# Performance work log

Hardware: AMD Instinct MI355X
Metric: run time of the kernel (lower is better)

Reference implementation:

```python
import jax, jax.numpy as jnp
import numpy as np

B, T, D, N = 16, 4096, 512, 3


def _window_sum(x, k):
    # x: [B, T, ...] -> sliding-window sum of size k, stride 1 -> [B, T-k+1, ...]
    c = jnp.cumsum(x, axis=1)
    c = jnp.concatenate([jnp.zeros_like(c[:, :1]), c], axis=1)
    return c[:, k:] - c[:, :-k]


def setup_inputs() -> dict:
    key = jax.random.key(0)
    ks = jax.random.split(key, 7)
    s_prev = jax.random.normal(ks[0], (B, D), jnp.float32)
    enc_hs = jax.random.normal(ks[1], (B, T, D), jnp.float32)
    # realistic padding mask: True = padded position
    lengths = jax.random.randint(ks[2], (B,), T // 2, T + 1)
    src_mask = jnp.arange(T)[None, :] >= lengths[:, None]
    scale = 1.0 / np.sqrt(D)
    Vw = jax.random.normal(ks[3], (N, D, D), jnp.float32) * scale
    Vb = jax.random.normal(ks[4], (N, D), jnp.float32) * 0.01
    Ww = jax.random.normal(ks[5], (N, D, D), jnp.float32) * scale
    Wb = jax.random.normal(ks[6], (N, D), jnp.float32) * 0.01
    return {"s_prev": s_prev, "enc_hs": enc_hs, "src_mask": src_mask,
            "Vw": Vw, "Vb": Vb, "Ww": Ww, "Wb": Wb}


def _level(s_prev, hs, mask, vw, vb, ww, wb):
    # hs: [B, L, D], mask: [B, L] (True = masked)
    # torch Linear: y = x @ W^T + b, weight is [out, in]
    v = jnp.einsum('bld,ed->ble', hs, vw) + vb            # V_i(hs)
    att = jnp.einsum('bd,bld->bl', s_prev, v)             # bmm(s_prev, V(hs)^T)
    att = jnp.where(mask, -jnp.inf, att)
    att = jax.nn.softmax(att, axis=-1)                    # [B, L]
    pooled = jnp.einsum('bl,bld->bd', att, hs)            # bmm(att, hs)
    ctx = pooled @ ww.T + wb                              # W_i(.)
    return ctx, att


def reference(s_prev, enc_hs, src_mask, Vw, Vb, Ww, Wb):
    ctx, att = _level(s_prev, enc_hs, src_mask, Vw[0], Vb[0], Ww[0], Wb[0])
    for i in range(1, N):
        k = i + 1
        hs_ngram = _window_sum(enc_hs, k) / k                      # AvgPool1d(k,1)
        n_mask = _window_sum(src_mask.astype(jnp.float32), k) > 0  # any masked in window
        c, _ = _level(s_prev, hs_ngram, n_mask, Vw[i], Vb[i], Ww[i], Wb[i])
        ctx = ctx + c
    return ctx, att
```

## Files before the change

kernel.cpp:

```cpp
#include <hip/hip_runtime.h>

#define BB 16
#define TT 4096
#define DD 512
#define CH 32
#define GR 4
#define NG (TT/(CH*GR))
#define NEG (-1.0e30f)

#define OFF_Q     64
#define OFF_QP    (OFF_Q + 3*BB*DD)
#define OFF_P0    (OFF_QP + 8*3*BB*DD)
#define OFF_M     (OFF_P0 + BB*TT)
#define OFF_S     (OFF_M + 3*BB*NG)
#define OFF_MT    (OFF_S + 3*BB*NG)
#define OFF_TOT   (OFF_MT + 64)
#define OFF_PART  (OFF_TOT + 64)
#define OFF_POOL  (OFF_PART + 3*NG*BB*DD)

__global__ void __launch_bounds__(256) k_pre(const unsigned char* __restrict__ mask,
                                             const float* __restrict__ s_prev,
                                             const float* __restrict__ Vw,
                                             int* __restrict__ lengths,
                                             float* __restrict__ qpart) {
    const int tid = threadIdx.x;
    if (blockIdx.x < BB) {
        __shared__ int sflag;
        __shared__ int wsum[4];
        const int b = blockIdx.x;
        if (tid == 0) sflag = 0;
        __syncthreads();
        const uint4* m4 = (const uint4*)mask;
        int f = 0;
        #pragma unroll 4
        for (int idx = tid; idx < BB * TT / 16; idx += 256) {
            const uint4 w = m4[idx];
            f |= (((w.x | w.y | w.z | w.w) & 0xFFFFFF00u) != 0u);
        }
        if (f) atomicOr(&sflag, 1);
        __syncthreads();
        const bool byte_layout = (sflag != 0);
        const int* m32 = (const int*)mask;
        int cnt = 0;
        if (byte_layout) {
            for (int t = tid; t < TT; t += 256) cnt += (mask[b * TT + t] != 0);
        } else {
            for (int t = tid; t < TT; t += 256) cnt += (m32[b * TT + t] != 0);
        }
        #pragma unroll
        for (int m = 32; m >= 1; m >>= 1) cnt += __shfl_xor(cnt, m, 64);
        if ((tid & 63) == 0) wsum[tid >> 6] = cnt;
        __syncthreads();
        if (tid == 0) lengths[b] = TT - (wsum[0] + wsum[1] + wsum[2] + wsum[3]);
    } else {
        __shared__ float4 red[2][128];
        const int idx = blockIdx.x - BB;
        const int ib = idx >> 3;
        const int ec = idx & 7;
        const int b = ib % BB;
        const int i = ib / BB;
        const int es = tid >> 7;
        const int dq = tid & 127;
        const int e0 = ec * 64 + es * 32;
        const float* sp = s_prev + b * DD + e0;
        const float4* W = (const float4*)(Vw + (size_t)i * DD * DD + (size_t)e0 * DD) + dq;
        float4 acc = make_float4(0.f, 0.f, 0.f, 0.f);
        #pragma unroll 8
        for (int e = 0; e < 32; e++) {
            const float sev = sp[e];
            const float4 w = W[e * 128];
            acc.x += sev * w.x; acc.y += sev * w.y;
            acc.z += sev * w.z; acc.w += sev * w.w;
        }
        red[es][dq] = acc;
        __syncthreads();
        if (tid < 128) {
            const float4 r0 = red[0][tid], r1 = red[1][tid];
            const float4 o = make_float4(r0.x + r1.x, r0.y + r1.y,
                                         r0.z + r1.z, r0.w + r1.w);
            ((float4*)(qpart + (size_t)idx * DD))[tid] = o;
        }
    }
}

__global__ void __launch_bounds__(256) k_q2(const float* __restrict__ qpart,
                                            float* __restrict__ q) {
    const int idx = blockIdx.x * 256 + threadIdx.x;
    const int ib = idx / DD;
    const int d = idx % DD;
    float s = 0.f;
    #pragma unroll
    for (int ec = 0; ec < 8; ec++) s += qpart[(size_t)(ib * 8 + ec) * DD + d];
    q[idx] = s;
}

__global__ void __launch_bounds__(512, 4) k_fused(const float* __restrict__ enc,
                                                  const float* __restrict__ q,
                                                  const int* __restrict__ lengths,
                                                  float* __restrict__ p0,
                                                  float* __restrict__ mbuf,
                                                  float* __restrict__ sbuf,
                                                  float* __restrict__ part) {
    __shared__ float se[CH + 2][DD];
    __shared__ float sp[CH + 2][3];
    __shared__ float su[3][CH];
    __shared__ float sms[3], sss[3];
    const int b = blockIdx.x;
    const int g = blockIdx.y;
    const int t0g = g * (CH * GR);
    const int len = lengths[b];
    const int tid = threadIdx.x;
    if (t0g >= len) {
        if (tid < 3) {
            mbuf[(size_t)(tid * BB + b) * NG + g] = NEG;
            sbuf[(size_t)(tid * BB + b) * NG + g] = 0.f;
        }
        return;
    }
    const int wv = tid >> 6, lane = tid & 63;

    const float4* q40 = (const float4*)(q + (size_t)(0 * BB + b) * DD);
    const float4* q41 = (const float4*)(q + (size_t)(1 * BB + b) * DD);
    const float4* q42 = (const float4*)(q + (size_t)(2 * BB + b) * DD);
    const float4 qa0 = q40[lane], qb0 = q40[64 + lane];
    const float4 qa1 = q41[lane], qb1 = q41[64 + lane];
    const float4 qa2 = q42[lane], qb2 = q42[64 + lane];

    float M0 = NEG, M1 = NEG, M2 = NEG;
    float S0 = 0.f, S1 = 0.f, S2 = 0.f;
    float A0 = 0.f, A1 = 0.f, A2 = 0.f;

    for (int sub = 0; sub < GR; sub++) {
        const int t0 = t0g + sub * CH;
        if (t0 >= len) break;
        if (sub) __syncthreads();

        auto row_task = [&](const int r, const bool wp0) {
            const int t = t0 + r;
            float4 x0 = make_float4(0.f, 0.f, 0.f, 0.f), x1 = x0;
            if (t < TT) {
                const float4* e4 = (const float4*)(enc + ((size_t)b * TT + t) * DD);
                x0 = e4[lane]; x1 = e4[64 + lane];
            }
            ((float4*)se[r])[lane] = x0;
            ((float4*)se[r])[64 + lane] = x1;
            float d0 = x0.x*qa0.x + x0.y*qa0.y + x0.z*qa0.z + x0.w*qa0.w
                     + x1.x*qb0.x + x1.y*qb0.y + x1.z*qb0.z + x1.w*qb0.w;
            float d1 = x0.x*qa1.x + x0.y*qa1.y + x0.z*qa1.z + x0.w*qa1.w
                     + x1.x*qb1.x + x1.y*qb1.y + x1.z*qb1.z + x1.w*qb1.w;
            float d2 = x0.x*qa2.x + x0.y*qa2.y + x0.z*qa2.z + x0.w*qa2.w
                     + x1.x*qb2.x + x1.y*qb2.y + x1.z*qb2.z + x1.w*qb2.w;
            #pragma unroll
            for (int m = 32; m >= 1; m >>= 1) {
                d0 += __shfl_xor(d0, m, 64);
                d1 += __shfl_xor(d1, m, 64);
                d2 += __shfl_xor(d2, m, 64);
            }
            if (lane == 0) {
                sp[r][0] = d0; sp[r][1] = d1; sp[r][2] = d2;
                if (wp0 && t < TT) p0[(size_t)b * TT + t] = d0;
            }
        };
        #pragma unroll
        for (int rr = 0; rr < 4; rr++) row_task(wv + rr * 8, true);
        if (wv < 2) row_task(CH + wv, false);
        __syncthreads();

        if (tid < 192) {
            const int i = wv;
            const bool act = lane < CH;
            const int r = lane & (CH - 1);
            const int l = t0 + r;
            const bool valid = act && (l < (len - i));
            float v = NEG;
            if (act) {
                float s = sp[r][i];
                if (i > 0) s += sp[r + 1][i];
                if (i > 1) s += sp[r + 2][i];
                const float kin = (i == 0) ? 1.0f : ((i == 1) ? 0.5f : (1.0f / 3.0f));
                v = valid ? s * kin : NEG;
            }
            float m = v;
            #pragma unroll
            for (int mm = 32; mm >= 1; mm >>= 1) m = fmaxf(m, __shfl_xor(m, mm, 64));
            const float u = valid ? __expf(v - m) : 0.f;
            if (act) su[i][r] = u;
            float ts = u;
            #pragma unroll
            for (int mm = 32; mm >= 1; mm >>= 1) ts += __shfl_xor(ts, mm, 64);
            if (lane == 0) { sms[i] = m; sss[i] = ts; }
        }
        __syncthreads();

        float va = se[0][tid], vb2 = se[1][tid];
        float a0 = 0.f, a1 = 0.f, a2 = 0.f;
        #pragma unroll
        for (int gg = 0; gg < CH / 4; gg++) {
            const float4 U0 = *(const float4*)&su[0][gg * 4];
            const float4 U1 = *(const float4*)&su[1][gg * 4];
            const float4 U2 = *(const float4*)&su[2][gg * 4];
            const float u0a[4] = {U0.x, U0.y, U0.z, U0.w};
            const float u1a[4] = {U1.x, U1.y, U1.z, U1.w};
            const float u2a[4] = {U2.x, U2.y, U2.z, U2.w};
            #pragma unroll
            for (int j = 0; j < 4; j++) {
                const float vc = se[gg * 4 + j + 2][tid];
                const float w1 = va + vb2;
                const float w2 = w1 + vc;
                a0 += u0a[j] * va;
                a1 += u1a[j] * w1;
                a2 += u2a[j] * w2;
                va = vb2; vb2 = vc;
            }
        }
        const float m0j = sms[0], m1j = sms[1], m2j = sms[2];
        const float s0j = sss[0], s1j = sss[1], s2j = sss[2];
        {
            const float nM = fmaxf(M0, m0j);
            const float so = __expf(M0 - nM), sn = __expf(m0j - nM);
            A0 = A0 * so + a0 * sn;  S0 = S0 * so + s0j * sn;  M0 = nM;
        }
        {
            const float nM = fmaxf(M1, m1j);
            const float so = __expf(M1 - nM), sn = __expf(m1j - nM);
            A1 = A1 * so + a1 * sn;  S1 = S1 * so + s1j * sn;  M1 = nM;
        }
        {
            const float nM = fmaxf(M2, m2j);
            const float so = __expf(M2 - nM), sn = __expf(m2j - nM);
            A2 = A2 * so + a2 * sn;  S2 = S2 * so + s2j * sn;  M2 = nM;
        }
    }
    A1 *= 0.5f; A2 *= (1.0f / 3.0f);
    float* pt = part + (size_t)g * BB * DD + (size_t)b * DD + tid;
    pt[0] = A0;
    pt[(size_t)NG * BB * DD] = A1;
    pt[(size_t)2 * NG * BB * DD] = A2;
    if (tid < 3) {
        const float Mv = (tid == 0) ? M0 : ((tid == 1) ? M1 : M2);
        const float Sv = (tid == 0) ? S0 : ((tid == 1) ? S1 : S2);
        mbuf[(size_t)(tid * BB + b) * NG + g] = Mv;
        sbuf[(size_t)(tid * BB + b) * NG + g] = Sv;
    }
}

__global__ void __launch_bounds__(256) k_reduce(const float* __restrict__ part,
                                                const float* __restrict__ mbuf,
                                                const float* __restrict__ sbuf,
                                                float* __restrict__ pooled,
                                                float* __restrict__ mtot,
                                                float* __restrict__ tot) {
    __shared__ float ssc[NG];
    const int blk = blockIdx.x;
    const int ib = blk >> 1;
    const int d = ((blk & 1) << 8) + threadIdx.x;
    const int i = ib / BB, b = ib % BB;
    if (threadIdx.x < 64) {
        const int lane = threadIdx.x;
        const bool a = lane < NG;
        const float ml = a ? mbuf[(size_t)ib * NG + lane] : NEG;
        const float sl = a ? sbuf[(size_t)ib * NG + lane] : 0.f;
        float m = ml;
        #pragma unroll
        for (int s = 32; s >= 1; s >>= 1) m = fmaxf(m, __shfl_xor(m, s, 64));
        float t = sl * __expf(ml - m);
        #pragma unroll
        for (int s = 32; s >= 1; s >>= 1) t += __shfl_xor(t, s, 64);
        const float inv = 1.0f / t;
        if (a) ssc[lane] = __expf(ml - m) * inv;
        if (lane == 0 && (blk & 1) == 0) { mtot[ib] = m; tot[ib] = t; }
    }
    __syncthreads();
    const float* base = part + (size_t)i * NG * BB * DD + (size_t)b * DD + d;
    float s = 0.f;
    #pragma unroll
    for (int yy = 0; yy < NG; yy++) {
        const float sc = ssc[yy];
        const float v = (sc != 0.f) ? base[(size_t)yy * BB * DD] : 0.f;
        s += v * sc;
    }
    pooled[(size_t)ib * DD + d] = s;
}

__global__ void __launch_bounds__(256) k_out(const float* __restrict__ pooled,
                                             const float* __restrict__ Ww,
                                             const float* __restrict__ Wb,
                                             const float* __restrict__ p0,
                                             const int* __restrict__ lengths,
                                             const float* __restrict__ mtot,
                                             const float* __restrict__ tot,
                                             float* __restrict__ ctx,
                                             float* __restrict__ att) {
    if (blockIdx.x < BB * DD / 4) {
        const int wid = blockIdx.x * 4 + (threadIdx.x >> 6);
        const int lane = threadIdx.x & 63;
        const int b = wid >> 9;
        const int e = wid & 511;
        float acc = 0.f;
        #pragma unroll
        for (int i = 0; i < 3; i++) {
            const float4* pr = (const float4*)(pooled + (size_t)(i * BB + b) * DD);
            const float4* wr = (const float4*)(Ww + ((size_t)i * DD + e) * DD);
            const float4 pA = pr[lane], pB = pr[64 + lane];
            const float4 wA = wr[lane], wB = wr[64 + lane];
            acc += pA.x * wA.x + pA.y * wA.y + pA.z * wA.z + pA.w * wA.w
                 + pB.x * wB.x + pB.y * wB.y + pB.z * wB.z + pB.w * wB.w;
        }
        #pragma unroll
        for (int m = 32; m >= 1; m >>= 1) acc += __shfl_xor(acc, m, 64);
        if (lane == 0)
            ctx[(size_t)b * DD + e] = acc + Wb[e] + Wb[DD + e] + Wb[2 * DD + e];
    } else {
        const int idx = (blockIdx.x - BB * DD / 4) * 256 + threadIdx.x;
        const int b = idx >> 12;
        const int t = idx & (TT - 1);
        att[idx] = (t < lengths[b]) ? __expf(p0[idx] - mtot[b]) * (1.0f / tot[b]) : 0.f;
    }
}

extern "C" void kernel_launch(void* const* d_in, const int* in_sizes, int n_in,
                              void* d_out, int out_size, void* d_ws, size_t ws_size,
                              hipStream_t stream) {
    const float* s_prev = (const float*)d_in[0];
    const float* enc    = (const float*)d_in[1];
    const void*  mask   = d_in[2];
    const float* Vw     = (const float*)d_in[3];
    const float* Ww     = (const float*)d_in[5];
    const float* Wb     = (const float*)d_in[6];

    float* out = (float*)d_out;
    float* ctx = out;
    float* att = out + BB * DD;

    float* W       = (float*)d_ws;
    int*   lengths = (int*)d_ws;
    float* q       = W + OFF_Q;
    float* qpart   = W + OFF_QP;
    float* p0      = W + OFF_P0;
    float* mbuf    = W + OFF_M;
    float* sbuf    = W + OFF_S;
    float* mtot    = W + OFF_MT;
    float* tot     = W + OFF_TOT;
    float* part    = W + OFF_PART;
    float* pooled  = W + OFF_POOL;

    k_pre<<<BB + 48 * 8, 256, 0, stream>>>((const unsigned char*)mask, s_prev, Vw,
                                           lengths, qpart);
    k_q2<<<3 * BB * DD / 256, 256, 0, stream>>>(qpart, q);
    k_fused<<<dim3(BB, NG), 512, 0, stream>>>(enc, q, lengths, p0, mbuf, sbuf, part);
    k_reduce<<<96, 256, 0, stream>>>(part, mbuf, sbuf, pooled, mtot, tot);
    k_out<<<BB * DD / 4 + BB * TT / 256, 256, 0, stream>>>(pooled, Ww, Wb, p0, lengths,
                                                           mtot, tot, ctx, att);
}
```

Baseline: 227.7 us.

## Interleave chunk assignment across blocks and reuse Ww rows across batches in output

The fused attention kernel now gives each block chunks strided by NG instead of a contiguous run. Under the variable padding lengths, this spreads valid work evenly across blocks rather than idling the blocks that cover the padded tail. The output projection now loads each Ww row once into registers and loops over all 16 batch rows, instead of re-reading the weights per batch. That cuts weight traffic but launches far fewer blocks for the GEMV portion, lengthening each block's serial loop.

```diff
diff --git a/kernel.cpp b/kernel.cpp
--- a/kernel.cpp
+++ b/kernel.cpp
@@ -107,16 +107,8 @@
     __shared__ float sms[3], sss[3];
     const int b = blockIdx.x;
     const int g = blockIdx.y;
-    const int t0g = g * (CH * GR);
     const int len = lengths[b];
     const int tid = threadIdx.x;
-    if (t0g >= len) {
-        if (tid < 3) {
-            mbuf[(size_t)(tid * BB + b) * NG + g] = NEG;
-            sbuf[(size_t)(tid * BB + b) * NG + g] = 0.f;
-        }
-        return;
-    }
     const int wv = tid >> 6, lane = tid & 63;
 
     const float4* q40 = (const float4*)(q + (size_t)(0 * BB + b) * DD);
@@ -130,10 +122,9 @@
     float S0 = 0.f, S1 = 0.f, S2 = 0.f;
     float A0 = 0.f, A1 = 0.f, A2 = 0.f;
 
-    for (int sub = 0; sub < GR; sub++) {
-        const int t0 = t0g + sub * CH;
-        if (t0 >= len) break;
-        if (sub) __syncthreads();
+    for (int j = 0; j < GR; j++) {
+        const int t0 = (g + j * NG) * CH;
+        if (t0 >= len) continue;
 
         auto row_task = [&](const int r, const bool wp0) {
             const int t = t0 + r;
@@ -203,13 +194,13 @@
             const float u1a[4] = {U1.x, U1.y, U1.z, U1.w};
             const float u2a[4] = {U2.x, U2.y, U2.z, U2.w};
             #pragma unroll
-            for (int j = 0; j < 4; j++) {
-                const float vc = se[gg * 4 + j + 2][tid];
+            for (int jj = 0; jj < 4; jj++) {
+                const float vc = se[gg * 4 + jj + 2][tid];
                 const float w1 = va + vb2;
                 const float w2 = w1 + vc;
-                a0 += u0a[j] * va;
-                a1 += u1a[j] * w1;
-                a2 += u2a[j] * w2;
+                a0 += u0a[jj] * va;
+                a1 += u1a[jj] * w1;
+                a2 += u2a[jj] * w2;
                 va = vb2; vb2 = vc;
             }
         }
@@ -230,6 +221,7 @@
             const float so = __expf(M2 - nM), sn = __expf(m2j - nM);
             A2 = A2 * so + a2 * sn;  S2 = S2 * so + s2j * sn;  M2 = nM;
         }
+        __syncthreads();
     }
     A1 *= 0.5f; A2 *= (1.0f / 3.0f);
     float* pt = part + (size_t)g * BB * DD + (size_t)b * DD + tid;
@@ -291,27 +283,35 @@
                                              const float* __restrict__ tot,
                                              float* __restrict__ ctx,
                                              float* __restrict__ att) {
-    if (blockIdx.x < BB * DD / 4) {
-        const int wid = blockIdx.x * 4 + (threadIdx.x >> 6);
-        const int lane = threadIdx.x & 63;
-        const int b = wid >> 9;
-        const int e = wid & 511;
-        float acc = 0.f;
-        #pragma unroll
-        for (int i = 0; i < 3; i++) {
-            const float4* pr = (const float4*)(pooled + (size_t)(i * BB + b) * DD);
-            const float4* wr = (const float4*)(Ww + ((size_t)i * DD + e) * DD);
-            const float4 pA = pr[lane], pB = pr[64 + lane];
-            const float4 wA = wr[lane], wB = wr[64 + lane];
-            acc += pA.x * wA.x + pA.y * wA.y + pA.z * wA.z + pA.w * wA.w
-                 + pB.x * wB.x + pB.y * wB.y + pB.z * wB.z + pB.w * wB.w;
-        }
-        #pragma unroll
-        for (int m = 32; m >= 1; m >>= 1) acc += __shfl_xor(acc, m, 64);
-        if (lane == 0)
-            ctx[(size_t)b * DD + e] = acc + Wb[e] + Wb[DD + e] + Wb[2 * DD + e];
+    const int lane = threadIdx.x & 63;
+    if (blockIdx.x < DD / 4) {
+        const int e = blockIdx.x * 4 + (threadIdx.x >> 6);
+        const float4* wr0 = (const float4*)(Ww + ((size_t)0 * DD + e) * DD);
+        const float4* wr1 = (const float4*)(Ww + ((size_t)1 * DD + e) * DD);
+        const float4* wr2 = (const float4*)(Ww + ((size_t)2 * DD + e) * DD);
+        const float4 w0A = wr0[lane], w0B = wr0[64 + lane];
+        const float4 w1A = wr1[lane], w1B = wr1[64 + lane];
+        const float4 w2A = wr2[lane], w2B = wr2[64 + lane];
+        const float bias = Wb[e] + Wb[DD + e] + Wb[2 * DD + e];
+        for (int b = 0; b < BB; b++) {
+            const float4* p0r = (const float4*)(pooled + (size_t)(0 * BB + b) * DD);
+            const float4* p1r = (const float4*)(pooled + (size_t)(1 * BB + b) * DD);
+            const float4* p2r = (const float4*)(pooled + (size_t)(2 * BB + b) * DD);
+            const float4 pA0 = p0r[lane], pB0 = p0r[64 + lane];
+            const float4 pA1 = p1r[lane], pB1 = p1r[64 + lane];
+            const float4 pA2 = p2r[lane], pB2 = p2r[64 + lane];
+            float acc = pA0.x*w0A.x + pA0.y*w0A.y + pA0.z*w0A.z + pA0.w*w0A.w
+                      + pB0.x*w0B.x + pB0.y*w0B.y + pB0.z*w0B.z + pB0.w*w0B.w
+                      + pA1.x*w1A.x + pA1.y*w1A.y + pA1.z*w1A.z + pA1.w*w1A.w
+                      + pB1.x*w1B.x + pB1.y*w1B.y + pB1.z*w1B.z + pB1.w*w1B.w
+                      + pA2.x*w2A.x + pA2.y*w2A.y + pA2.z*w2A.z + pA2.w*w2A.w
+                      + pB2.x*w2B.x + pB2.y*w2B.y + pB2.z*w2B.z + pB2.w*w2B.w;
+            #pragma unroll
+            for (int m = 32; m >= 1; m >>= 1) acc += __shfl_xor(acc, m, 64);
+            if (lane == 0) ctx[(size_t)b * DD + e] = acc + bias;
+        }
     } else {
-        const int idx = (blockIdx.x - BB * DD / 4) * 256 + threadIdx.x;
+        const int idx = (blockIdx.x - DD / 4) * 256 + threadIdx.x;
         const int b = idx >> 12;
         const int t = idx & (TT - 1);
         att[idx] = (t < lengths[b]) ? __expf(p0[idx] - mtot[b]) * (1.0f / tot[b]) : 0.f;
@@ -349,6 +349,6 @@
     k_q2<<<3 * BB * DD / 256, 256, 0, stream>>>(qpart, q);
     k_fused<<<dim3(BB, NG), 512, 0, stream>>>(enc, q, lengths, p0, mbuf, sbuf, part);
     k_reduce<<<96, 256, 0, stream>>>(part, mbuf, sbuf, pooled, mtot, tot);
-    k_out<<<BB * DD / 4 + BB * TT / 256, 256, 0, stream>>>(pooled, Ww, Wb, p0, lengths,
-                                                           mtot, tot, ctx, att);
-}
+    k_out<<<DD / 4 + BB * TT / 256, 256, 0, stream>>>(pooled, Ww, Wb, p0, lengths,
+                                                      mtot, tot, ctx, att);
+}
```

Result: slower. 238.0 us (+4.5%).
